# Kernel tuning notes

Hardware: AMD Instinct MI355X
Metric: run time of the kernel (lower is better)

## Reference

```python
import jax, jax.numpy as jnp
import numpy as np

SCALE = 64.0   # CosFace scale s
MARGIN = 0.35  # CosFace margin m
EPS = 1e-12


def setup_inputs() -> dict:
    key = jax.random.key(0)
    k1, k2, k3 = jax.random.split(key, 3)
    batch, feat_dim, num_classes = 512, 512, 100000
    return {
        "input": jax.random.normal(k1, (batch, feat_dim), dtype=jnp.float32),
        "label": jax.random.randint(k2, (batch,), 0, num_classes, dtype=jnp.int64),
        "w": jax.random.normal(k3, (feat_dim, num_classes), dtype=jnp.float32),
    }


def reference(input, label, w):
    # L2-normalize features (rows) and class weights (columns), as in _forward_train
    feat_norm = jnp.clip(jnp.linalg.norm(input, axis=1, keepdims=True), EPS, None)
    normed_feat = input / feat_norm                      # [B, D]
    w_norm = jnp.clip(jnp.linalg.norm(w, axis=0, keepdims=True), EPS, None)
    normed_w = w / w_norm                                # [D, C]
    cosine = jnp.clip(normed_feat @ normed_w, -1.0, 1.0)  # [B, C]
    # CosFace margin applied at the true-label position (get_probs_i)
    onehot = jax.nn.one_hot(label, w.shape[1], dtype=cosine.dtype)
    logits = SCALE * (cosine - MARGIN * onehot)          # [B, C]
    # loss = mean(logsumexp over all (sharded) classes - logit at true label)
    lse = jax.nn.logsumexp(logits, axis=1)               # [B]
    x = jnp.take_along_axis(logits, label[:, None], axis=1)[:, 0]  # [B]
    return jnp.mean(lse - x)
```

## Files before the change

kernel.cpp:

```cpp
#include <hip/hip_runtime.h>
#include <hip/hip_bf16.h>
#include <math.h>

#define BDIM 512
#define DDIM 512
#define CDIM 100000
#define NC 64
#define BM 128
#define BN 128
#define BK 32
#define NKSTEP (DDIM / BK)
#define GNB 782
#define CPADT 100096
#define NCHT (CPADT / NC)
#define NBLK (GNB * 4)
#define CTILE 128

typedef __attribute__((ext_vector_type(8))) short short8;
typedef __attribute__((ext_vector_type(4))) float f32x4;

__device__ __forceinline__ unsigned short f2bf(float f) {
  unsigned int u = __builtin_bit_cast(unsigned int, f);
  u = (u + 0x7FFFu + ((u >> 16) & 1u)) >> 16;
  return (unsigned short)u;
}

__device__ __forceinline__ void gl_lds16(const unsigned short* g, unsigned short* l) {
  __builtin_amdgcn_global_load_lds(
      (const __attribute__((address_space(1))) void*)g,
      (__attribute__((address_space(3))) void*)l, 16, 0, 0);
}

__global__ void k_rownorm(const float* __restrict__ x, unsigned short* __restrict__ a) {
  const int b = blockIdx.x;
  const int tid = threadIdx.x;
  const float* row = x + (size_t)b * DDIM;
  float v0 = row[tid], v1 = row[tid + 256];
  float ss = v0 * v0 + v1 * v1;
  #pragma unroll
  for (int m = 1; m < 64; m <<= 1) ss += __shfl_xor(ss, m);
  __shared__ float sred[4];
  __shared__ float sinv;
  if ((tid & 63) == 0) sred[tid >> 6] = ss;
  __syncthreads();
  if (tid == 0) {
    float s = sred[0] + sred[1] + sred[2] + sred[3];
    sinv = 1.f / fmaxf(sqrtf(s), 1e-12f);
  }
  __syncthreads();
  const float inv = sinv;
  a[(size_t)b * DDIM + tid] = f2bf(v0 * inv);
  a[(size_t)b * DDIM + tid + 256] = f2bf(v1 * inv);
}

__global__ __launch_bounds__(512)
void k_wt(const float* __restrict__ w, unsigned short* __restrict__ wt,
          float* __restrict__ invwn) {
  __shared__ float tile[64][CTILE + 4];
  const int t = threadIdx.x;
  const int c0w = blockIdx.x * CTILE;
  const int rd_d = t >> 3;
  const int rd_c = (t & 7) * 16;
  const int wc = t >> 2;
  const int wh = t & 3;
  float ss = 0.f;

  for (int ch = 0; ch < 8; ch++) {
    const int d0 = ch * 64;
    float4 r[4];
    #pragma unroll
    for (int j = 0; j < 4; j++) {
      const int c = c0w + rd_c + j * 4;
      if (c + 3 < CDIM)
        r[j] = *reinterpret_cast<const float4*>(w + (size_t)(d0 + rd_d) * CDIM + c);
      else {
        #pragma unroll
        for (int e = 0; e < 4; e++)
          r[j][e] = (c + e < CDIM) ? w[(size_t)(d0 + rd_d) * CDIM + c + e] : 0.f;
      }
    }
    #pragma unroll
    for (int j = 0; j < 4; j++)
      *reinterpret_cast<float4*>(&tile[rd_d][rd_c + j * 4]) = r[j];
    __syncthreads();

    short8 o0, o1;
    #pragma unroll
    for (int j = 0; j < 8; j++) {
      const float v = tile[wh * 16 + j][wc];
      ss += v * v;
      o0[j] = (short)f2bf(v);
    }
    #pragma unroll
    for (int j = 0; j < 8; j++) {
      const float v = tile[wh * 16 + 8 + j][wc];
      ss += v * v;
      o1[j] = (short)f2bf(v);
    }
    {
      unsigned short* dst = wt + ((size_t)(c0w + wc) << 9) + d0 + wh * 16;
      *reinterpret_cast<short8*>(dst) = o0;
      *reinterpret_cast<short8*>(dst + 8) = o1;
    }
    __syncthreads();
  }
  ss += __shfl_xor(ss, 1);
  ss += __shfl_xor(ss, 2);
  if (wh == 0)
    invwn[c0w + wc] = (c0w + wc < CDIM) ? 1.f / fmaxf(sqrtf(ss), 1e-12f) : 1.f;
}

__global__ __launch_bounds__(256, 4)
void k_main(const unsigned short* __restrict__ a,
            const unsigned short* __restrict__ wt,
            const float* __restrict__ invwn,
            const long long* __restrict__ label,
            float2* __restrict__ part,
            float* __restrict__ labellogit) {
  __shared__ __align__(16) unsigned short alds[2][BM * BK];
  __shared__ __align__(16) unsigned short blds[2][BN * BK];

  const int t = threadIdx.x;
  const int orig = (blockIdx.x & 7) * (NBLK / 8) + (blockIdx.x >> 3);
  const int rb = orig & 3;
  const int cb = orig >> 2;
  const int bm0 = rb * BM;
  const int bn0 = cb * BN;

  const int wave = t >> 6;
  const int lane = t & 63;
  const int wr = wave >> 1;
  const int wc = wave & 1;
  const int lhi = lane >> 4;
  const int llo = lane & 15;

  auto stage = [&](int s, int buf) {
    #pragma unroll
    for (int i = 0; i < 2; i++) {
      const int r = wave * 32 + i * 16 + (lane >> 2);
      const int piece = (lane & 3) ^ ((r >> 1) & 3);
      gl_lds16(a + (size_t)(bm0 + r) * DDIM + s * BK + piece * 8,
               &alds[buf][(wave * 32 + i * 16) * BK]);
      gl_lds16(wt + ((size_t)(bn0 + r) << 9) + s * BK + piece * 8,
               &blds[buf][(wave * 32 + i * 16) * BK]);
    }
  };

  f32x4 acc[4][4];
  #pragma unroll
  for (int i = 0; i < 4; i++)
    #pragma unroll
    for (int j = 0; j < 4; j++)
      acc[i][j] = (f32x4){0.f, 0.f, 0.f, 0.f};

  stage(0, 0);
  __syncthreads();

  #pragma unroll
  for (int s = 0; s < NKSTEP; s++) {
    if (s + 1 < NKSTEP) stage(s + 1, (s + 1) & 1);

    const int buf = s & 1;
    short8 af[4], bfr[4];
    #pragma unroll
    for (int m = 0; m < 4; m++) {
      const int row = wr * 64 + m * 16 + llo;
      const int pc = lhi ^ ((row >> 1) & 3);
      af[m] = *reinterpret_cast<const short8*>(&alds[buf][row * BK + pc * 8]);
    }
    #pragma unroll
    for (int n = 0; n < 4; n++) {
      const int col = wc * 64 + n * 16 + llo;
      const int pc = lhi ^ ((col >> 1) & 3);
      bfr[n] = *reinterpret_cast<const short8*>(&blds[buf][col * BK + pc * 8]);
    }
    #pragma unroll
    for (int m = 0; m < 4; m++)
      #pragma unroll
      for (int n = 0; n < 4; n++)
        acc[m][n] = __builtin_amdgcn_mfma_f32_16x16x32_bf16(af[m], bfr[n], acc[m][n], 0, 0, 0);

    __syncthreads();
  }

  float inv[4];
  #pragma unroll
  for (int n = 0; n < 4; n++)
    inv[n] = invwn[bn0 + wc * 64 + n * 16 + llo];

  const int chunk = cb * 2 + wc;
  #pragma unroll
  for (int m = 0; m < 4; m++) {
    #pragma unroll
    for (int r = 0; r < 4; r++) {
      const int row = bm0 + wr * 64 + m * 16 + (lhi << 2) + r;
      const int lab = (int)label[row];
      float vals[4];
      float mloc = -100.0f;
      #pragma unroll
      for (int n = 0; n < 4; n++) {
        const int cg = bn0 + wc * 64 + n * 16 + llo;
        float cs = acc[m][n][r] * inv[n];
        cs = fminf(fmaxf(cs, -1.f), 1.f);
        float lg = 64.f * cs;
        if (cg == lab) { lg = 64.f * (cs - 0.35f); labellogit[row] = lg; }
        if (cg >= CDIM) lg = -INFINITY;
        vals[n] = lg;
        mloc = fmaxf(mloc, lg);
      }
      float mm = mloc;
      #pragma unroll
      for (int msk = 1; msk < 16; msk <<= 1) mm = fmaxf(mm, __shfl_xor(mm, msk));
      float sacc = 0.f;
      #pragma unroll
      for (int n = 0; n < 4; n++) sacc += __expf(vals[n] - mm);
      #pragma unroll
      for (int msk = 1; msk < 16; msk <<= 1) sacc += __shfl_xor(sacc, msk);
      if (llo == 0) part[(size_t)chunk * BDIM + row] = make_float2(mm, sacc);
    }
  }
}

__global__ void k_rowreduce(const float2* __restrict__ part,
                            const float* __restrict__ labellogit,
                            float* __restrict__ rowloss) {
  const int row = blockIdx.x;
  const int tid = threadIdx.x;
  float m = -INFINITY, s = 0.f;
  for (int ch = tid; ch < NCHT; ch += 256) {
    float2 p = part[(size_t)ch * BDIM + row];
    float nm = fmaxf(m, p.x);
    s = s * __expf(m - nm) + p.y * __expf(p.x - nm);
    m = nm;
  }
  #pragma unroll
  for (int msk = 1; msk < 64; msk <<= 1) {
    float om = __shfl_xor(m, msk), os = __shfl_xor(s, msk);
    float nm = fmaxf(m, om);
    s = s * __expf(m - nm) + os * __expf(om - nm);
    m = nm;
  }
  __shared__ float sm[4], ssum[4];
  const int wv = tid >> 6, ln = tid & 63;
  if (ln == 0) { sm[wv] = m; ssum[wv] = s; }
  __syncthreads();
  if (tid == 0) {
    float M = sm[0], S = ssum[0];
    #pragma unroll
    for (int i = 1; i < 4; i++) {
      float nm = fmaxf(M, sm[i]);
      S = S * __expf(M - nm) + ssum[i] * __expf(sm[i] - nm);
      M = nm;
    }
    rowloss[row] = M + logf(S) - labellogit[row];
  }
}

__global__ void k_mean(const float* __restrict__ rowloss, float* __restrict__ out) {
  const int tid = threadIdx.x;
  float v = rowloss[tid];
  #pragma unroll
  for (int msk = 1; msk < 64; msk <<= 1) v += __shfl_xor(v, msk);
  __shared__ float sred[8];
  if ((tid & 63) == 0) sred[tid >> 6] = v;
  __syncthreads();
  if (tid == 0) {
    float s = 0.f;
    #pragma unroll
    for (int i = 0; i < 8; i++) s += sred[i];
    out[0] = s / (float)BDIM;
  }
}

extern "C" void kernel_launch(void* const* d_in, const int* in_sizes, int n_in,
                              void* d_out, int out_size, void* d_ws, size_t ws_size,
                              hipStream_t stream) {
  const float* input = (const float*)d_in[0];
  const long long* label = (const long long*)d_in[1];
  const float* w = (const float*)d_in[2];
  float* out = (float*)d_out;

  char* ws = (char*)d_ws;
  unsigned short* a_bf16 = (unsigned short*)(ws + 0);
  float2* part           = (float2*)(ws + 524288);
  float* labellogit      = (float*)(ws + 6930432);
  float* rowloss         = (float*)(ws + 6932480);
  float* invwn           = (float*)(ws + 6934528);
  unsigned short* w_t    = (unsigned short*)(ws + 7334912);

  k_rownorm<<<BDIM, 256, 0, stream>>>(input, a_bf16);
  k_wt<<<CPADT / CTILE, 512, 0, stream>>>(w, w_t, invwn);
  k_main<<<NBLK, 256, 0, stream>>>(a_bf16, w_t, invwn, label, part, labellogit);
  k_rowreduce<<<BDIM, 256, 0, stream>>>(part, labellogit, rowloss);
  k_mean<<<1, BDIM, 0, stream>>>(rowloss, out);
}
```

Measured before the change: 181.6 us.

## Load GEMM fragments directly from global memory, dropping LDS staging

Removes the double-buffered LDS staging of A and W tiles, which used global_load_lds with swizzling. Each wave now reads its MFMA operand fragments straight from global memory through per-row pointers. This drops the LDS traffic and the per-step barriers. In exchange each tile is fetched redundantly by both waves that share it, so the kernel leans on L1/L2 hit rates and loses explicit prefetch overlap.

```diff
diff --git a/kernel.cpp b/kernel.cpp
--- a/kernel.cpp
+++ b/kernel.cpp
@@ -8,8 +8,7 @@
 #define NC 64
 #define BM 128
 #define BN 128
-#define BK 32
-#define NKSTEP (DDIM / BK)
+#define NKSTEP 16
 #define GNB 782
 #define CPADT 100096
 #define NCHT (CPADT / NC)
@@ -23,12 +22,6 @@
   unsigned int u = __builtin_bit_cast(unsigned int, f);
   u = (u + 0x7FFFu + ((u >> 16) & 1u)) >> 16;
   return (unsigned short)u;
-}
-
-__device__ __forceinline__ void gl_lds16(const unsigned short* g, unsigned short* l) {
-  __builtin_amdgcn_global_load_lds(
-      (const __attribute__((address_space(1))) void*)g,
-      (__attribute__((address_space(3))) void*)l, 16, 0, 0);
 }
 
 __global__ void k_rownorm(const float* __restrict__ x, unsigned short* __restrict__ a) {
@@ -117,9 +110,6 @@
             const long long* __restrict__ label,
             float2* __restrict__ part,
             float* __restrict__ labellogit) {
-  __shared__ __align__(16) unsigned short alds[2][BM * BK];
-  __shared__ __align__(16) unsigned short blds[2][BN * BK];
-
   const int t = threadIdx.x;
   const int orig = (blockIdx.x & 7) * (NBLK / 8) + (blockIdx.x >> 3);
   const int rb = orig & 3;
@@ -134,17 +124,14 @@
   const int lhi = lane >> 4;
   const int llo = lane & 15;
 
-  auto stage = [&](int s, int buf) {
-    #pragma unroll
-    for (int i = 0; i < 2; i++) {
-      const int r = wave * 32 + i * 16 + (lane >> 2);
-      const int piece = (lane & 3) ^ ((r >> 1) & 3);
-      gl_lds16(a + (size_t)(bm0 + r) * DDIM + s * BK + piece * 8,
-               &alds[buf][(wave * 32 + i * 16) * BK]);
-      gl_lds16(wt + ((size_t)(bn0 + r) << 9) + s * BK + piece * 8,
-               &blds[buf][(wave * 32 + i * 16) * BK]);
-    }
-  };
+  const unsigned short* ab[4];
+  const unsigned short* bb[4];
+  #pragma unroll
+  for (int m = 0; m < 4; m++)
+    ab[m] = a + (size_t)(bm0 + wr * 64 + m * 16 + llo) * DDIM + (lhi << 3);
+  #pragma unroll
+  for (int n = 0; n < 4; n++)
+    bb[n] = wt + ((size_t)(bn0 + wc * 64 + n * 16 + llo) << 9) + (lhi << 3);
 
   f32x4 acc[4][4];
   #pragma unroll
@@ -153,34 +140,21 @@
     for (int j = 0; j < 4; j++)
       acc[i][j] = (f32x4){0.f, 0.f, 0.f, 0.f};
 
-  stage(0, 0);
-  __syncthreads();
-
   #pragma unroll
   for (int s = 0; s < NKSTEP; s++) {
-    if (s + 1 < NKSTEP) stage(s + 1, (s + 1) & 1);
-
-    const int buf = s & 1;
-    short8 af[4], bfr[4];
-    #pragma unroll
-    for (int m = 0; m < 4; m++) {
-      const int row = wr * 64 + m * 16 + llo;
-      const int pc = lhi ^ ((row >> 1) & 3);
-      af[m] = *reinterpret_cast<const short8*>(&alds[buf][row * BK + pc * 8]);
-    }
-    #pragma unroll
-    for (int n = 0; n < 4; n++) {
-      const int col = wc * 64 + n * 16 + llo;
-      const int pc = lhi ^ ((col >> 1) & 3);
-      bfr[n] = *reinterpret_cast<const short8*>(&blds[buf][col * BK + pc * 8]);
-    }
+    const int koff = s * 32;
+    short8 af[4], bf[4];
     #pragma unroll
     for (int m = 0; m < 4; m++)
+      af[m] = *reinterpret_cast<const short8*>(ab[m] + koff);
+    #pragma unroll
+    for (int n = 0; n < 4; n++)
+      bf[n] = *reinterpret_cast<const short8*>(bb[n] + koff);
+    #pragma unroll
+    for (int m = 0; m < 4; m++)
       #pragma unroll
       for (int n = 0; n < 4; n++)
-        acc[m][n] = __builtin_amdgcn_mfma_f32_16x16x32_bf16(af[m], bfr[n], acc[m][n], 0, 0, 0);
-
-    __syncthreads();
+        acc[m][n] = __builtin_amdgcn_mfma_f32_16x16x32_bf16(af[m], bf[n], acc[m][n], 0, 0, 0);
   }
 
   float inv[4];
```

New measurement: 305.7 us. 1.68x slower.
